# Kernel optimization log

Hardware: AMD Instinct MI355X
Metric: run time of the kernel (lower is better)

Reference implementation:

```python
import jax, jax.numpy as jnp
import numpy as np

B = 64          # batch
H = 768         # hidden_size
K = 65536       # queue_size
NUM_LABELS = 64
TOP_K = 25      # knn_num
T = 0.5         # temperature
RATE = 0.5      # contrastive_rate_in_training
POS_MIN = K // NUM_LABELS          # balanced queue -> static pos count per row
NEG_MIN = K - POS_MIN
NEG_TOPK = min(POS_MIN, TOP_K)     # = TOP_K here


def l2norm(x):
    return x / jnp.sqrt(jnp.sum(x * x, axis=-1, keepdims=True))


def setup_inputs() -> dict:
    key = jax.random.key(0)
    ks = jax.random.split(key, 8)
    q = jax.random.normal(ks[0], (B, H), dtype=jnp.float32)
    labels = jax.random.randint(ks[1], (B,), 0, NUM_LABELS - 1)  # CE over num_labels-1 classes
    # exactly-balanced label queue so pos_min/neg_min are static (matches torch math)
    label_queue = jnp.arange(K, dtype=jnp.int64) % NUM_LABELS
    fq = jax.random.normal(ks[2], (K, H), dtype=jnp.float32)
    fq = fq / jnp.linalg.norm(fq, axis=0, keepdims=True)  # torch normalizes dim=0
    s = 0.02
    return {
        "q": q,
        "labels": labels,
        "label_queue": label_queue,
        "feature_queue": fq,
        "Wd": s * jax.random.normal(ks[3], (H, H), dtype=jnp.float32),
        "bd": jnp.zeros((H,), jnp.float32),
        "Wo": s * jax.random.normal(ks[4], (H, H), dtype=jnp.float32),
        "bo": jnp.zeros((H,), jnp.float32),
        "Wc1": s * jax.random.normal(ks[5], (H, H), dtype=jnp.float32),
        "bc1": jnp.zeros((H,), jnp.float32),
        "Wc2": s * jax.random.normal(ks[6], (H, NUM_LABELS - 1), dtype=jnp.float32),
        "bc2": jnp.zeros((NUM_LABELS - 1,), jnp.float32),
    }


def cross_entropy(logits, labels):
    logp = jax.nn.log_softmax(logits, axis=-1)
    return -jnp.mean(jnp.take_along_axis(logp, labels[:, None], axis=-1))


def reference(q, labels, label_queue, feature_queue, Wd, bd, Wo, bo, Wc1, bc1, Wc2, bc2):
    # contrastive head (dropout is identity at eval)
    liner_q = l2norm(jnp.tanh(q @ Wd + bd) @ Wo + bo)                 # [B,H]
    # classification head + CE over (num_labels-1) classes
    logits_cls = jnp.tanh(q @ Wc1 + bc1) @ Wc2 + bc2                  # [B,L-1]
    loss_cls = cross_entropy(logits_cls, labels)

    # select_pos_neg_sample: cosine sim vs queue (repeat in torch is redundant)
    cos_sim = liner_q @ feature_queue.T                               # [B,K]
    pos_mask = labels[:, None] == label_queue[None, :]                # [B,K]

    # positives: topk of raw cos_sim (as in torch code), keep first TOP_K
    pos_sample, _ = jax.lax.top_k(cos_sim, POS_MIN)                   # [B,POS_MIN]
    pos_sample = pos_sample[:, :TOP_K].reshape(-1, 1)                 # [B*TOP_K,1]

    # negatives: mask positives to -inf, topk NEG_MIN (all finite: queue balanced)
    neg = jnp.where(pos_mask, -jnp.inf, cos_sim)                      # [B,K]
    neg_sample, _ = jax.lax.top_k(neg, NEG_MIN)                       # [B,NEG_MIN]
    neg_rep = jnp.broadcast_to(neg_sample[:, None, :], (B, NEG_TOPK, NEG_MIN))
    neg_rep = neg_rep.reshape(-1, NEG_MIN)                            # [B*TOP_K,NEG_MIN]

    logits_con = jnp.concatenate([pos_sample, neg_rep], axis=-1) / T  # [B*TOP_K,1+NEG_MIN]
    # labels_con = 0 -> NLL of column 0
    loss_con = -jnp.mean(jax.nn.log_softmax(logits_con, axis=-1)[:, 0])

    loss = loss_con * RATE + loss_cls * (1.0 - RATE)
    return loss
```

## Files before the change

kernel.cpp:

```cpp
#include <hip/hip_runtime.h>
#include <hip/hip_bf16.h>
#include <math.h>

#define HH 768
#define KK 65536
#define NCLS 63
#define TOPK 25

typedef short short8v __attribute__((ext_vector_type(8)));
typedef float f32x4 __attribute__((ext_vector_type(4)));

static __device__ __forceinline__ short f2bf(float x) {
    __hip_bfloat16 h = __float2bfloat16(x);
    return *reinterpret_cast<short*>(&h);
}

#define P1_OFF 0
#define P2_OFF 196608
#define P3_OFF 393216
#define CLS_OFF 589824
#define CON_OFF 589888
#define CSUM_OFF 589952
#define CTOP_OFF 590464
#define LQB_OFF 0
#define COS_OFF 615680
#define PSTRIDE 49152

__global__ __launch_bounds__(256) void gemm_qk_part(const float* __restrict__ q,
                                                    const float* __restrict__ Wd,
                                                    const float* __restrict__ Wc1,
                                                    float* __restrict__ ws) {
    const int g  = blockIdx.x / 96;
    const int r  = blockIdx.x % 96;
    const int ct = r >> 2, kc = r & 3;
    const float* W = g ? Wc1 : Wd;
    float* P = ws + (g ? P2_OFF : P1_OFF) + kc * PSTRIDE;
    __shared__ float xs[64][32];
    const int c  = ct * 32 + (threadIdx.x & 31);
    const int rg = threadIdx.x >> 5;
    float acc[8];
#pragma unroll
    for (int i = 0; i < 8; i++) acc[i] = 0.f;
    for (int k0 = kc * 192; k0 < kc * 192 + 192; k0 += 32) {
        for (int i = threadIdx.x; i < 64 * 32; i += 256)
            xs[i >> 5][i & 31] = q[(i >> 5) * HH + k0 + (i & 31)];
        __syncthreads();
#pragma unroll 8
        for (int kk = 0; kk < 32; kk++) {
            float w = W[(size_t)(k0 + kk) * HH + c];
#pragma unroll
            for (int i = 0; i < 8; i++) acc[i] += xs[rg + 8 * i][kk] * w;
        }
        __syncthreads();
    }
#pragma unroll
    for (int i = 0; i < 8; i++) P[(rg + 8 * i) * HH + c] = acc[i];
}

__global__ __launch_bounds__(256) void gemm3_cls(const float* __restrict__ ws_ro,
                                                 const float* __restrict__ bd,
                                                 const float* __restrict__ Wo,
                                                 const float* __restrict__ bc1,
                                                 const float* __restrict__ Wc2,
                                                 const float* __restrict__ bc2,
                                                 const int* __restrict__ labels,
                                                 float* __restrict__ ws) {
    if (blockIdx.x < 96) {
        const int ct = blockIdx.x >> 2, kc = blockIdx.x & 3;
        float* P = ws + P3_OFF + kc * PSTRIDE;
        __shared__ float xs[64][32];
        const int c  = ct * 32 + (threadIdx.x & 31);
        const int rg = threadIdx.x >> 5;
        float acc[8];
#pragma unroll
        for (int i = 0; i < 8; i++) acc[i] = 0.f;
        for (int k0 = kc * 192; k0 < kc * 192 + 192; k0 += 32) {
            for (int i = threadIdx.x; i < 64 * 32; i += 256) {
                int rr = i >> 5, kk = i & 31, k = k0 + kk;
                float v = ws_ro[P1_OFF + 0 * PSTRIDE + rr * HH + k]
                        + ws_ro[P1_OFF + 1 * PSTRIDE + rr * HH + k]
                        + ws_ro[P1_OFF + 2 * PSTRIDE + rr * HH + k]
                        + ws_ro[P1_OFF + 3 * PSTRIDE + rr * HH + k] + bd[k];
                xs[rr][kk] = tanhf(v);
            }
            __syncthreads();
#pragma unroll 8
            for (int kk = 0; kk < 32; kk++) {
                float w = Wo[(size_t)(k0 + kk) * HH + c];
#pragma unroll
                for (int i = 0; i < 8; i++) acc[i] += xs[rg + 8 * i][kk] * w;
            }
            __syncthreads();
        }
#pragma unroll
        for (int i = 0; i < 8; i++) P[(rg + 8 * i) * HH + c] = acc[i];
    } else {
        const int b = blockIdx.x - 96;
        __shared__ float t2s[HH];
        __shared__ float psum[4][64];
        for (int h = threadIdx.x; h < HH; h += 256) {
            float v = ws_ro[P2_OFF + 0 * PSTRIDE + b * HH + h]
                    + ws_ro[P2_OFF + 1 * PSTRIDE + b * HH + h]
                    + ws_ro[P2_OFF + 2 * PSTRIDE + b * HH + h]
                    + ws_ro[P2_OFF + 3 * PSTRIDE + b * HH + h] + bc1[h];
            t2s[h] = tanhf(v);
        }
        __syncthreads();
        const int c  = threadIdx.x & 63;
        const int kq = threadIdx.x >> 6;
        float a = 0.f;
        if (c < NCLS) {
            for (int h = kq * 192; h < kq * 192 + 192; h++)
                a += t2s[h] * Wc2[h * NCLS + c];
        }
        psum[kq][c] = a;
        __syncthreads();
        if (threadIdx.x < 64) {
            float logit = (c < NCLS)
                ? psum[0][c] + psum[1][c] + psum[2][c] + psum[3][c] + bc2[c]
                : -INFINITY;
            float m = logit;
            for (int o = 32; o > 0; o >>= 1) m = fmaxf(m, __shfl_xor(m, o));
            float e = (c < NCLS) ? __expf(logit - m) : 0.f;
            for (int o = 32; o > 0; o >>= 1) e += __shfl_xor(e, o);
            float lse = m + logf(e);
            float lv = __shfl(logit, labels[b]);
            if (threadIdx.x == 0) ws[CLS_OFF + b] = lse - lv;
        }
    }
}

__global__ __launch_bounds__(256) void l2norm_bf16(const float* __restrict__ ws_ro,
                                                   const float* __restrict__ bo,
                                                   float* __restrict__ ws) {
    __shared__ float red[4];
    __shared__ float inv_s;
    const int b = blockIdx.x;
    short* out = (short*)(ws + LQB_OFF);
    float s = 0.f;
    for (int h = threadIdx.x; h < HH; h += 256) {
        float v = ws_ro[P3_OFF + 0 * PSTRIDE + b * HH + h]
                + ws_ro[P3_OFF + 1 * PSTRIDE + b * HH + h]
                + ws_ro[P3_OFF + 2 * PSTRIDE + b * HH + h]
                + ws_ro[P3_OFF + 3 * PSTRIDE + b * HH + h] + bo[h];
        s += v * v;
    }
    for (int o = 32; o > 0; o >>= 1) s += __shfl_down(s, o);
    if ((threadIdx.x & 63) == 0) red[threadIdx.x >> 6] = s;
    __syncthreads();
    if (threadIdx.x == 0) inv_s = rsqrtf(red[0] + red[1] + red[2] + red[3]);
    __syncthreads();
    float inv = inv_s;
    for (int h = threadIdx.x; h < HH; h += 256) {
        float v = ws_ro[P3_OFF + 0 * PSTRIDE + b * HH + h]
                + ws_ro[P3_OFF + 1 * PSTRIDE + b * HH + h]
                + ws_ro[P3_OFF + 2 * PSTRIDE + b * HH + h]
                + ws_ro[P3_OFF + 3 * PSTRIDE + b * HH + h] + bo[h];
        out[b * HH + h] = f2bf(v * inv);
    }
}

__global__ __launch_bounds__(256) void cos_mfma(const float* __restrict__ ws_ro,
                                                const float* __restrict__ FQ,
                                                float* __restrict__ ws) {
    const short* LQb = (const short*)(ws_ro + LQB_OFF);
    float* cosv = ws + COS_OFF;
    const int wave = threadIdx.x >> 6;
    const int lane = threadIdx.x & 63;
    const int lr = lane & 15;
    const int lg = lane >> 4;
    const int n0 = (blockIdx.x * 4 + wave) * 16;
    f32x4 acc[4];
#pragma unroll
    for (int m = 0; m < 4; m++) acc[m] = (f32x4){0.f, 0.f, 0.f, 0.f};
    const float* fq = FQ + (size_t)(n0 + lr) * HH + lg * 8;
    const short* aq = LQb + lr * HH + lg * 8;
    for (int h0 = 0; h0 < HH; h0 += 32) {
        f32x4 b0 = *(const f32x4*)(fq + h0);
        f32x4 b1 = *(const f32x4*)(fq + h0 + 4);
        short8v bfr;
        bfr[0] = f2bf(b0[0]); bfr[1] = f2bf(b0[1]); bfr[2] = f2bf(b0[2]); bfr[3] = f2bf(b0[3]);
        bfr[4] = f2bf(b1[0]); bfr[5] = f2bf(b1[1]); bfr[6] = f2bf(b1[2]); bfr[7] = f2bf(b1[3]);
#pragma unroll
        for (int m = 0; m < 4; m++) {
            short8v afr = *(const short8v*)(aq + m * 16 * HH + h0);
            acc[m] = __builtin_amdgcn_mfma_f32_16x16x32_bf16(afr, bfr, acc[m], 0, 0, 0);
        }
    }
#pragma unroll
    for (int m = 0; m < 4; m++)
#pragma unroll
        for (int i = 0; i < 4; i++)
            cosv[(size_t)(m * 16 + lg * 4 + i) * KK + n0 + lr] = acc[m][i];
}

__global__ __launch_bounds__(256) void reduce1(const float* __restrict__ ws_ro,
                                               const int* __restrict__ labels,
                                               float* __restrict__ ws) {
    const float* cosv = ws_ro + COS_OFF;
    float* chunk_top = ws + CTOP_OFF;
    float* chunk_sum = ws + CSUM_OFF;
    const int b = blockIdx.x >> 3;
    const int c = blockIdx.x & 7;
    const int tid = threadIdx.x;
    __shared__ float cand[256 * TOPK];
    __shared__ float wv[4];
    __shared__ int wi[4];
    const int lab = labels[b];
    const bool neg = ((tid & 63) != lab);
    const float* row = cosv + (size_t)b * KK + c * 8192;
    float* my = cand + tid * TOPK;
    float s = 0.f;
    for (int i = 0; i < TOPK; i++) {
        float v = row[i * 256 + tid];
        if (neg) s += __expf(2.f * v);
        my[i] = v;
    }
    float vmin = my[0]; int mi = 0;
#pragma unroll
    for (int t = 1; t < TOPK; t++) if (my[t] < vmin) { vmin = my[t]; mi = t; }
    for (int i = TOPK; i < 32; i++) {
        float v = row[i * 256 + tid];
        if (neg) s += __expf(2.f * v);
        if (v > vmin) {
            my[mi] = v;
            vmin = my[0]; mi = 0;
#pragma unroll
            for (int t = 1; t < TOPK; t++) if (my[t] < vmin) { vmin = my[t]; mi = t; }
        }
    }
    for (int o = 32; o > 0; o >>= 1) s += __shfl_down(s, o);
    if ((tid & 63) == 0) wv[tid >> 6] = s;
    __syncthreads();
    if (tid == 0) chunk_sum[b * 8 + c] = wv[0] + wv[1] + wv[2] + wv[3];
    __syncthreads();
    for (int it = 0; it < TOPK; it++) {
        float bvv = my[0]; int bs = 0;
#pragma unroll
        for (int t = 1; t < TOPK; t++) if (my[t] > bvv) { bvv = my[t]; bs = t; }
        int ci = tid * TOPK + bs;
        for (int o = 32; o > 0; o >>= 1) {
            float ov = __shfl_down(bvv, o); int oc = __shfl_down(ci, o);
            if (ov > bvv) { bvv = ov; ci = oc; }
        }
        if ((tid & 63) == 0) { wv[tid >> 6] = bvv; wi[tid >> 6] = ci; }
        __syncthreads();
        if (tid == 0) {
            float xv = wv[0]; int xi = wi[0];
            for (int w = 1; w < 4; w++) if (wv[w] > xv) { xv = wv[w]; xi = wi[w]; }
            chunk_top[(size_t)(b * 8 + c) * TOPK + it] = xv;
            cand[xi] = -INFINITY;
        }
        __syncthreads();
    }
}

__global__ __launch_bounds__(64) void reduce2(const float* __restrict__ ws_ro,
                                              float* __restrict__ ws) {
    const float* chunk_top = ws_ro + CTOP_OFF;
    const float* chunk_sum = ws_ro + CSUM_OFF;
    __shared__ float topv[TOPK];
    const int b = blockIdx.x;
    const int lane = threadIdx.x;
    float S = 0.f;
#pragma unroll
    for (int c = 0; c < 8; c++) S += chunk_sum[b * 8 + c];
    float v[4];
#pragma unroll
    for (int j = 0; j < 4; j++) {
        int g = j * 64 + lane;
        v[j] = (g < 200) ? chunk_top[(size_t)b * 200 + g] : -INFINITY;
    }
    for (int it = 0; it < TOPK; it++) {
        float bv = v[0]; int bj = 0;
#pragma unroll
        for (int j = 1; j < 4; j++) if (v[j] > bv) { bv = v[j]; bj = j; }
        int gid = bj * 64 + lane;
        for (int o = 32; o > 0; o >>= 1) {
            float ov = __shfl_xor(bv, o); int og = __shfl_xor(gid, o);
            if (ov > bv || (ov == bv && og < gid)) { bv = ov; gid = og; }
        }
#pragma unroll
        for (int j = 0; j < 4; j++) if (gid == j * 64 + lane) v[j] = -INFINITY;
        if (lane == 0) topv[it] = bv;
    }
    __syncthreads();
    float part = 0.f;
    if (lane < TOPK) {
        float p2 = 2.f * topv[lane];
        part = logf(__expf(p2) + S) - p2;
    }
    for (int o = 32; o > 0; o >>= 1) part += __shfl_down(part, o);
    if (lane == 0) ws[CON_OFF + b] = part;
}

__global__ __launch_bounds__(64) void finalize(const float* __restrict__ ws_ro,
                                               float* __restrict__ out) {
    const int t = threadIdx.x;
    float c = ws_ro[CLS_OFF + t];
    float p = ws_ro[CON_OFF + t];
    for (int o = 32; o > 0; o >>= 1) { c += __shfl_down(c, o); p += __shfl_down(p, o); }
    if (t == 0) out[0] = 0.5f * (p / (64.f * 25.f)) + 0.5f * (c / 64.f);
}

extern "C" void kernel_launch(void* const* d_in, const int* in_sizes, int n_in,
                              void* d_out, int out_size, void* d_ws, size_t ws_size,
                              hipStream_t stream) {
    const float* q      = (const float*)d_in[0];
    const int*   labels = (const int*)d_in[1];
    const float* fq  = (const float*)d_in[3];
    const float* Wd  = (const float*)d_in[4];
    const float* bd  = (const float*)d_in[5];
    const float* Wo  = (const float*)d_in[6];
    const float* bo  = (const float*)d_in[7];
    const float* Wc1 = (const float*)d_in[8];
    const float* bc1 = (const float*)d_in[9];
    const float* Wc2 = (const float*)d_in[10];
    const float* bc2 = (const float*)d_in[11];

    float* ws = (float*)d_ws;

    gemm_qk_part<<<192, 256, 0, stream>>>(q, Wd, Wc1, ws);
    gemm3_cls<<<160, 256, 0, stream>>>(ws, bd, Wo, bc1, Wc2, bc2, labels, ws);
    l2norm_bf16<<<64, 256, 0, stream>>>(ws, bo, ws);
    cos_mfma<<<1024, 256, 0, stream>>>(ws, fq, ws);
    reduce1<<<512, 256, 0, stream>>>(ws, labels, ws);
    reduce2<<<64, 64, 0, stream>>>(ws, ws);
    finalize<<<1, 64, 0, stream>>>(ws, (float*)d_out);
}
```

Baseline: 466.6 us.

## Move head GEMMs to bf16 MFMA with pre-transposed weights

Replaces the scalar fp32 split-K GEMMs for the contrastive and classification heads with bf16 MFMA kernels. A new prep kernel converts q to bf16 and transposes the Wd, Wc1 and Wo weights into bf16. Bias and tanh are fused into the GEMM epilogues, which removes the split-K partial buffers and their reductions. The cost is an extra transpose pass over roughly 1.7M weight elements on every call, plus bf16 rounding in the head projections.

```diff
diff --git a/kernel.cpp b/kernel.cpp
--- a/kernel.cpp
+++ b/kernel.cpp
@@ -15,96 +15,132 @@
     return *reinterpret_cast<short*>(&h);
 }
 
-#define P1_OFF 0
-#define P2_OFF 196608
-#define P3_OFF 393216
-#define CLS_OFF 589824
-#define CON_OFF 589888
-#define CSUM_OFF 589952
-#define CTOP_OFF 590464
-#define LQB_OFF 0
-#define COS_OFF 615680
-#define PSTRIDE 49152
-
-__global__ __launch_bounds__(256) void gemm_qk_part(const float* __restrict__ q,
-                                                    const float* __restrict__ Wd,
-                                                    const float* __restrict__ Wc1,
-                                                    float* __restrict__ ws) {
-    const int g  = blockIdx.x / 96;
-    const int r  = blockIdx.x % 96;
-    const int ct = r >> 2, kc = r & 3;
-    const float* W = g ? Wc1 : Wd;
-    float* P = ws + (g ? P2_OFF : P1_OFF) + kc * PSTRIDE;
-    __shared__ float xs[64][32];
-    const int c  = ct * 32 + (threadIdx.x & 31);
-    const int rg = threadIdx.x >> 5;
-    float acc[8];
-#pragma unroll
-    for (int i = 0; i < 8; i++) acc[i] = 0.f;
-    for (int k0 = kc * 192; k0 < kc * 192 + 192; k0 += 32) {
-        for (int i = threadIdx.x; i < 64 * 32; i += 256)
-            xs[i >> 5][i & 31] = q[(i >> 5) * HH + k0 + (i & 31)];
-        __syncthreads();
-#pragma unroll 8
-        for (int kk = 0; kk < 32; kk++) {
-            float w = W[(size_t)(k0 + kk) * HH + c];
-#pragma unroll
-            for (int i = 0; i < 8; i++) acc[i] += xs[rg + 8 * i][kk] * w;
-        }
-        __syncthreads();
-    }
-#pragma unroll
-    for (int i = 0; i < 8; i++) P[(rg + 8 * i) * HH + c] = acc[i];
-}
-
-__global__ __launch_bounds__(256) void gemm3_cls(const float* __restrict__ ws_ro,
-                                                 const float* __restrict__ bd,
-                                                 const float* __restrict__ Wo,
-                                                 const float* __restrict__ bc1,
+#define QB_OFF   0
+#define WDT_OFF  24576
+#define WC1T_OFF 319488
+#define WOT_OFF  614400
+#define T1B_OFF  909312
+#define T2_OFF   933888
+#define Y_OFF    983040
+#define CLS_OFF  1032192
+#define CON_OFF  1032256
+#define CSUM_OFF 1032320
+#define CTOP_OFF 1032832
+#define LQB_OFF  1045632
+#define COS_OFF  1070208
+
+__global__ __launch_bounds__(256) void prep(const float* __restrict__ q,
+                                            const float* __restrict__ Wd,
+                                            const float* __restrict__ Wc1,
+                                            const float* __restrict__ Wo,
+                                            float* __restrict__ ws) {
+    if (blockIdx.x < 3) {
+        short* qb = (short*)(ws + QB_OFF);
+        const int g = blockIdx.x * 256 + threadIdx.x;
+        for (int i = 0; i < 64; i++) qb[i * HH + g] = f2bf(q[i * HH + g]);
+    } else {
+        __shared__ short ls[32][33];
+        const int tile0 = (blockIdx.x - 3) * 4;
+        const int r8 = threadIdx.x >> 5, c = threadIdx.x & 31;
+        for (int tt = 0; tt < 4; tt++) {
+            const int tile = tile0 + tt;
+            const int mat = tile / 576, rem = tile % 576;
+            const int tr = rem / 24, tc = rem % 24;
+            const float* W = mat == 0 ? Wd : (mat == 1 ? Wc1 : Wo);
+            short* WT = (short*)(ws + (mat == 0 ? WDT_OFF : (mat == 1 ? WC1T_OFF : WOT_OFF)));
+            __syncthreads();
+#pragma unroll
+            for (int j = 0; j < 4; j++)
+                ls[r8 + j * 8][c] = f2bf(W[(size_t)(tr * 32 + r8 + j * 8) * HH + tc * 32 + c]);
+            __syncthreads();
+#pragma unroll
+            for (int j = 0; j < 4; j++)
+                WT[(size_t)(tc * 32 + r8 + j * 8) * HH + tr * 32 + c] = ls[c][r8 + j * 8];
+        }
+    }
+}
+
+__global__ __launch_bounds__(256) void head1(const float* __restrict__ ws_ro,
+                                             const float* __restrict__ bd,
+                                             const float* __restrict__ bc1,
+                                             float* __restrict__ ws) {
+    const short* qb = (const short*)(ws_ro + QB_OFF);
+    const int wave = threadIdx.x >> 6, lane = threadIdx.x & 63;
+    const int lr = lane & 15, lg = lane >> 4;
+    const int wt = blockIdx.x * 4 + wave;
+    const int mat = wt / 48;
+    const int n0 = (wt % 48) * 16;
+    const short* BT = (const short*)(ws_ro + (mat ? WC1T_OFF : WDT_OFF));
+    f32x4 acc[4];
+#pragma unroll
+    for (int m = 0; m < 4; m++) acc[m] = (f32x4){0.f, 0.f, 0.f, 0.f};
+    const short* bq = BT + (size_t)(n0 + lr) * HH + lg * 8;
+    const short* aq = qb + lr * HH + lg * 8;
+    for (int h0 = 0; h0 < HH; h0 += 32) {
+        short8v bfr = *(const short8v*)(bq + h0);
+#pragma unroll
+        for (int m = 0; m < 4; m++) {
+            short8v afr = *(const short8v*)(aq + m * 16 * HH + h0);
+            acc[m] = __builtin_amdgcn_mfma_f32_16x16x32_bf16(afr, bfr, acc[m], 0, 0, 0);
+        }
+    }
+    if (mat == 0) {
+        short* T1b = (short*)(ws + T1B_OFF);
+        float bv = bd[n0 + lr];
+#pragma unroll
+        for (int m = 0; m < 4; m++)
+#pragma unroll
+            for (int i = 0; i < 4; i++)
+                T1b[(m * 16 + lg * 4 + i) * HH + n0 + lr] = f2bf(tanhf(acc[m][i] + bv));
+    } else {
+        float* T2 = ws + T2_OFF;
+        float bv = bc1[n0 + lr];
+#pragma unroll
+        for (int m = 0; m < 4; m++)
+#pragma unroll
+            for (int i = 0; i < 4; i++)
+                T2[(m * 16 + lg * 4 + i) * HH + n0 + lr] = tanhf(acc[m][i] + bv);
+    }
+}
+
+__global__ __launch_bounds__(256) void head2_cls(const float* __restrict__ ws_ro,
+                                                 const float* __restrict__ bo,
                                                  const float* __restrict__ Wc2,
                                                  const float* __restrict__ bc2,
                                                  const int* __restrict__ labels,
                                                  float* __restrict__ ws) {
-    if (blockIdx.x < 96) {
-        const int ct = blockIdx.x >> 2, kc = blockIdx.x & 3;
-        float* P = ws + P3_OFF + kc * PSTRIDE;
-        __shared__ float xs[64][32];
-        const int c  = ct * 32 + (threadIdx.x & 31);
-        const int rg = threadIdx.x >> 5;
-        float acc[8];
-#pragma unroll
-        for (int i = 0; i < 8; i++) acc[i] = 0.f;
-        for (int k0 = kc * 192; k0 < kc * 192 + 192; k0 += 32) {
-            for (int i = threadIdx.x; i < 64 * 32; i += 256) {
-                int rr = i >> 5, kk = i & 31, k = k0 + kk;
-                float v = ws_ro[P1_OFF + 0 * PSTRIDE + rr * HH + k]
-                        + ws_ro[P1_OFF + 1 * PSTRIDE + rr * HH + k]
-                        + ws_ro[P1_OFF + 2 * PSTRIDE + rr * HH + k]
-                        + ws_ro[P1_OFF + 3 * PSTRIDE + rr * HH + k] + bd[k];
-                xs[rr][kk] = tanhf(v);
+    if (blockIdx.x < 12) {
+        const short* T1b = (const short*)(ws_ro + T1B_OFF);
+        const short* BT  = (const short*)(ws_ro + WOT_OFF);
+        const int wave = threadIdx.x >> 6, lane = threadIdx.x & 63;
+        const int lr = lane & 15, lg = lane >> 4;
+        const int n0 = (blockIdx.x * 4 + wave) * 16;
+        f32x4 acc[4];
+#pragma unroll
+        for (int m = 0; m < 4; m++) acc[m] = (f32x4){0.f, 0.f, 0.f, 0.f};
+        const short* bq = BT + (size_t)(n0 + lr) * HH + lg * 8;
+        const short* aq = T1b + lr * HH + lg * 8;
+        for (int h0 = 0; h0 < HH; h0 += 32) {
+            short8v bfr = *(const short8v*)(bq + h0);
+#pragma unroll
+            for (int m = 0; m < 4; m++) {
+                short8v afr = *(const short8v*)(aq + m * 16 * HH + h0);
+                acc[m] = __builtin_amdgcn_mfma_f32_16x16x32_bf16(afr, bfr, acc[m], 0, 0, 0);
             }
-            __syncthreads();
-#pragma unroll 8
-            for (int kk = 0; kk < 32; kk++) {
-                float w = Wo[(size_t)(k0 + kk) * HH + c];
-#pragma unroll
-                for (int i = 0; i < 8; i++) acc[i] += xs[rg + 8 * i][kk] * w;
-            }
-            __syncthreads();
-        }
-#pragma unroll
-        for (int i = 0; i < 8; i++) P[(rg + 8 * i) * HH + c] = acc[i];
+        }
+        float* Y = ws + Y_OFF;
+        float bv = bo[n0 + lr];
+#pragma unroll
+        for (int m = 0; m < 4; m++)
+#pragma unroll
+            for (int i = 0; i < 4; i++)
+                Y[(m * 16 + lg * 4 + i) * HH + n0 + lr] = acc[m][i] + bv;
     } else {
-        const int b = blockIdx.x - 96;
+        const int b = blockIdx.x - 12;
+        const float* T2 = ws_ro + T2_OFF;
         __shared__ float t2s[HH];
         __shared__ float psum[4][64];
-        for (int h = threadIdx.x; h < HH; h += 256) {
-            float v = ws_ro[P2_OFF + 0 * PSTRIDE + b * HH + h]
-                    + ws_ro[P2_OFF + 1 * PSTRIDE + b * HH + h]
-                    + ws_ro[P2_OFF + 2 * PSTRIDE + b * HH + h]
-                    + ws_ro[P2_OFF + 3 * PSTRIDE + b * HH + h] + bc1[h];
-            t2s[h] = tanhf(v);
-        }
+        for (int h = threadIdx.x; h < HH; h += 256) t2s[h] = T2[b * HH + h];
         __syncthreads();
         const int c  = threadIdx.x & 63;
         const int kq = threadIdx.x >> 6;
@@ -131,33 +167,22 @@
 }
 
 __global__ __launch_bounds__(256) void l2norm_bf16(const float* __restrict__ ws_ro,
-                                                   const float* __restrict__ bo,
                                                    float* __restrict__ ws) {
     __shared__ float red[4];
     __shared__ float inv_s;
     const int b = blockIdx.x;
+    const float* Y = ws_ro + Y_OFF;
     short* out = (short*)(ws + LQB_OFF);
     float s = 0.f;
-    for (int h = threadIdx.x; h < HH; h += 256) {
-        float v = ws_ro[P3_OFF + 0 * PSTRIDE + b * HH + h]
-                + ws_ro[P3_OFF + 1 * PSTRIDE + b * HH + h]
-                + ws_ro[P3_OFF + 2 * PSTRIDE + b * HH + h]
-                + ws_ro[P3_OFF + 3 * PSTRIDE + b * HH + h] + bo[h];
-        s += v * v;
-    }
+    for (int h = threadIdx.x; h < HH; h += 256) { float v = Y[b * HH + h]; s += v * v; }
     for (int o = 32; o > 0; o >>= 1) s += __shfl_down(s, o);
     if ((threadIdx.x & 63) == 0) red[threadIdx.x >> 6] = s;
     __syncthreads();
     if (threadIdx.x == 0) inv_s = rsqrtf(red[0] + red[1] + red[2] + red[3]);
     __syncthreads();
     float inv = inv_s;
-    for (int h = threadIdx.x; h < HH; h += 256) {
-        float v = ws_ro[P3_OFF + 0 * PSTRIDE + b * HH + h]
-                + ws_ro[P3_OFF + 1 * PSTRIDE + b * HH + h]
-                + ws_ro[P3_OFF + 2 * PSTRIDE + b * HH + h]
-                + ws_ro[P3_OFF + 3 * PSTRIDE + b * HH + h] + bo[h];
-        out[b * HH + h] = f2bf(v * inv);
-    }
+    for (int h = threadIdx.x; h < HH; h += 256)
+        out[b * HH + h] = f2bf(Y[b * HH + h] * inv);
 }
 
 __global__ __launch_bounds__(256) void cos_mfma(const float* __restrict__ ws_ro,
@@ -320,9 +345,10 @@
 
     float* ws = (float*)d_ws;
 
-    gemm_qk_part<<<192, 256, 0, stream>>>(q, Wd, Wc1, ws);
-    gemm3_cls<<<160, 256, 0, stream>>>(ws, bd, Wo, bc1, Wc2, bc2, labels, ws);
-    l2norm_bf16<<<64, 256, 0, stream>>>(ws, bo, ws);
+    prep<<<435, 256, 0, stream>>>(q, Wd, Wc1, Wo, ws);
+    head1<<<24, 256, 0, stream>>>(ws, bd, bc1, ws);
+    head2_cls<<<76, 256, 0, stream>>>(ws, bo, Wc2, bc2, labels, ws);
+    l2norm_bf16<<<64, 256, 0, stream>>>(ws, ws);
     cos_mfma<<<1024, 256, 0, stream>>>(ws, fq, ws);
     reduce1<<<512, 256, 0, stream>>>(ws, labels, ws);
     reduce2<<<64, 64, 0, stream>>>(ws, ws);
```

Measured after the change: 413.2 us. 1.13x faster.
